# Optimization experiments

Hardware: AMD Instinct MI355X
Metric: run time of the kernel (lower is better)

Reference implementation:

```python
import jax, jax.numpy as jnp
import numpy as np

NUM_STEPS = 2  # consensus iterations


def psi3(r, edge_index, W3, b3):
    # one-layer message passing GNN: sum-aggregate neighbors, add self, linear, relu
    src, dst = edge_index[0], edge_index[1]
    agg = jnp.zeros_like(r).at[dst].add(r[src])
    return jax.nn.relu((r + agg) @ W3 + b3)


def setup_inputs() -> dict:
    key = jax.random.key(0)
    ks = jax.random.split(key, 12)
    N_total, C_in = 4096, 128   # global entity table
    N_s, N_t = 1024, 1024       # source / target graph sizes (B=1)
    E = 16384                   # edges per graph (avg degree 16)
    C1, C2 = 256, 256           # psi_1 / psi_2 output dims
    R = 32                      # psi_3 in_channels == out_channels
    s_in = 1.0 / np.sqrt(C_in)
    s_r = 1.0 / np.sqrt(R)
    inp = {}
    inp['inputs'] = jax.random.normal(ks[0], (N_total, C_in), jnp.float32)
    inp['index_n1'] = jax.random.randint(ks[1], (N_s,), 0, N_total)
    inp['index_n2'] = jax.random.randint(ks[2], (N_t,), 0, N_total)
    inp['edge_index_s'] = jax.random.randint(ks[3], (2, E), 0, N_s)
    inp['edge_index_t'] = jax.random.randint(ks[4], (2, E), 0, N_t)
    # psi_1 / psi_2: linear entity encoders
    inp['W1'] = jax.random.uniform(ks[5], (C_in, C1), jnp.float32, -s_in, s_in)
    inp['W2'] = jax.random.uniform(ks[6], (C_in, C2), jnp.float32, -s_in, s_in)
    # psi_3 weights
    inp['W3'] = jax.random.uniform(ks[7], (R, R), jnp.float32, -s_r, s_r)
    inp['b3'] = jnp.zeros((R,), jnp.float32)
    # consensus MLP: R -> R -> 1
    inp['Wm1'] = jax.random.uniform(ks[8], (R, R), jnp.float32, -s_r, s_r)
    inp['bm1'] = jnp.zeros((R,), jnp.float32)
    inp['Wm2'] = jax.random.uniform(ks[9], (R, 1), jnp.float32, -s_r, s_r)
    inp['bm2'] = jnp.zeros((1,), jnp.float32)
    # random node indicator functions r_s for each consensus step (drawn
    # with torch.randn inside the original forward; precomputed here)
    inp['rs_all'] = jax.random.normal(ks[10], (NUM_STEPS, N_s, R), jnp.float32)
    return inp


def reference(inputs, index_n1, index_n2, edge_index_s, edge_index_t,
              W1, W2, W3, b3, Wm1, bm1, Wm2, bm2, rs_all):
    time_emb = inputs @ W1  # psi_1
    rel_emb = inputs @ W2   # psi_2
    # h = cat(time, rel) per node; B=1 so masks are all-true
    h_s = jnp.concatenate([time_emb[index_n1], rel_emb[index_n1]], axis=-1)  # [N_s, C1+C2]
    h_t = jnp.concatenate([time_emb[index_n2], rel_emb[index_n2]], axis=-1)  # [N_t, C1+C2]
    S_hat = h_s @ h_t.T  # [N_s, N_t] dense similarity
    S_0 = jax.nn.softmax(S_hat, axis=-1)  # masked_softmax with full mask

    def step(S_hat, r_s):
        S = jax.nn.softmax(S_hat, axis=-1)
        r_t = S.T @ r_s                                  # [N_t, R]
        o_s = psi3(r_s, edge_index_s, W3, b3)            # [N_s, R]
        o_t = psi3(r_t, edge_index_t, W3, b3)            # [N_t, R]
        D = o_s[:, None, :] - o_t[None, :, :]            # [N_s, N_t, R]
        delta = (jax.nn.relu(D @ Wm1 + bm1) @ Wm2 + bm2)[..., 0]  # mlp(D).squeeze(-1)
        return S_hat + delta, None

    S_hat, _ = jax.lax.scan(step, S_hat, rs_all)
    S_L = jax.nn.softmax(S_hat, axis=-1)
    return S_0, S_L
```

## Files before the change

kernel.cpp:

```cpp
#include <hip/hip_runtime.h>
#include <math.h>

#define N_S   1024
#define N_T   1024
#define C_IN  128
#define E_EDG 16384
#define R     32
#define NSTEP 2

__global__ __launch_bounds__(256) void k_pre(const float* __restrict__ W1,
                                             const float* __restrict__ W2,
                                             float* __restrict__ G,
                                             float* __restrict__ zbuf) {
    int t = threadIdx.x;
    ((float4*)zbuf)[blockIdx.x * 256 + t] = make_float4(0.f, 0.f, 0.f, 0.f);

    int a = blockIdx.x;
    __shared__ float wa[512];
    __shared__ float wt[64][129];
    __shared__ float red[256];
    for (int s = t; s < 512; s += 256)
        wa[s] = (s < 256) ? W1[a * 256 + s] : W2[a * 256 + (s - 256)];
    __syncthreads();

    float acc = 0.f;
    int b = t & 127, h = t >> 7;
    for (int ci = 0; ci < 8; ++ci) {
        const float* Wsrc = (ci < 4) ? W1 : W2;
        int cbase = (ci < 4) ? ci * 64 : (ci - 4) * 64;
#pragma unroll
        for (int it = 0; it < 8; ++it) {
            int s = it * 256 + t;
            int br = s >> 4, q = s & 15;
            float4 v = *(const float4*)(Wsrc + (size_t)br * 256 + cbase + q * 4);
            wt[q * 4 + 0][br] = v.x; wt[q * 4 + 1][br] = v.y;
            wt[q * 4 + 2][br] = v.z; wt[q * 4 + 3][br] = v.w;
        }
        __syncthreads();
        const float* wac = wa + ci * 64 + h * 32;
#pragma unroll
        for (int cc = 0; cc < 32; ++cc)
            acc += wac[cc] * wt[h * 32 + cc][b];
        __syncthreads();
    }
    red[t] = acc;
    __syncthreads();
    if (t < 128) G[a * 128 + t] = red[t] + red[t + 128];
}

__global__ __launch_bounds__(128) void k_ys(const float* __restrict__ X,
                                            const int* __restrict__ idx1,
                                            const float* __restrict__ G,
                                            float* __restrict__ Ys) {
    int i = blockIdx.x;
    int a = threadIdx.x;
    __shared__ float x[128];
    int row = idx1[i];
    x[a] = X[row * 128 + a];
    __syncthreads();
    float acc = 0.f;
#pragma unroll 8
    for (int d = 0; d < 128; ++d)
        acc += x[d] * G[d * 128 + a];
    Ys[i * 128 + a] = acc;
}

__global__ __launch_bounds__(256) void k_shat(const float* __restrict__ Ys,
                                              const float* __restrict__ X,
                                              const int* __restrict__ idx2,
                                              float* __restrict__ Shat,
                                              float2* __restrict__ part) {
    __shared__ float As[64][132];
    __shared__ float Bs[64][132];
    const int i0 = blockIdx.y * 64, j0 = blockIdx.x * 64;
    const int t = threadIdx.x;
    for (int s = t; s < 64 * 32; s += 256) {
        int row = s >> 5, q = s & 31;
        float4 v = ((const float4*)(Ys + (size_t)(i0 + row) * 128))[q];
        *(float4*)&As[row][q * 4] = v;
    }
    for (int s = t; s < 64 * 32; s += 256) {
        int row = s >> 5, q = s & 31;
        int src = idx2[j0 + row];
        float4 v = ((const float4*)(X + (size_t)src * 128))[q];
        *(float4*)&Bs[row][q * 4] = v;
    }
    __syncthreads();
    const int r = t >> 4, c = t & 15;
    float acc[4][4] = {};
    for (int k = 0; k < 128; k += 4) {
        float4 ya[4], xb[4];
#pragma unroll
        for (int a = 0; a < 4; ++a) ya[a] = *(const float4*)&As[r + 16 * a][k];
#pragma unroll
        for (int b = 0; b < 4; ++b) xb[b] = *(const float4*)&Bs[c + 16 * b][k];
#pragma unroll
        for (int a = 0; a < 4; ++a)
#pragma unroll
            for (int b = 0; b < 4; ++b)
                acc[a][b] += ya[a].x * xb[b].x + ya[a].y * xb[b].y +
                             ya[a].z * xb[b].z + ya[a].w * xb[b].w;
    }
#pragma unroll
    for (int a = 0; a < 4; ++a) {
#pragma unroll
        for (int b = 0; b < 4; ++b)
            Shat[(size_t)(i0 + r + 16 * a) * 1024 + (j0 + c + 16 * b)] = acc[a][b];
        float M = fmaxf(fmaxf(acc[a][0], acc[a][1]), fmaxf(acc[a][2], acc[a][3]));
#pragma unroll
        for (int m = 1; m < 16; m <<= 1) M = fmaxf(M, __shfl_xor(M, m, 16));
        float Ss = 0.f;
#pragma unroll
        for (int b = 0; b < 4; ++b) Ss += __expf(acc[a][b] - M);
#pragma unroll
        for (int m = 1; m < 16; m <<= 1) Ss += __shfl_xor(Ss, m, 16);
        if (c == 0)
            part[(size_t)(i0 + r + 16 * a) * 16 + blockIdx.x] = make_float2(M, Ss);
    }
}

__global__ __launch_bounds__(256) void k_scat_s(const int* __restrict__ es,
                                                const float* __restrict__ rs_all,
                                                float* __restrict__ aggs0,
                                                float* __restrict__ aggs1) {
    int gid = blockIdx.x * 256 + threadIdx.x;
    int k = gid & 31;
    int ei = gid >> 5;
    int step = ei >> 14;
    int e = ei & (E_EDG - 1);
    int src = es[e], dst = es[E_EDG + e];
    const float* rs = rs_all + (size_t)step * N_S * R;
    float* aggs = step ? aggs1 : aggs0;
    atomicAdd(&aggs[(size_t)dst * 32 + k], rs[(size_t)src * 32 + k]);
}

__global__ __launch_bounds__(256) void k_post_s(const float* __restrict__ rs_all,
                                                const float* __restrict__ aggs0,
                                                const float* __restrict__ aggs1,
                                                const float* __restrict__ W3,
                                                const float* __restrict__ b3,
                                                const float* __restrict__ Wm1,
                                                const float* __restrict__ bm1,
                                                float* __restrict__ P0,
                                                float* __restrict__ P1) {
    __shared__ float w3[1024], wm1[1024];
    __shared__ float ul[8][33], ol[8][33];
    int t = threadIdx.x;
    for (int s = t; s < 1024; s += 256) { w3[s] = W3[s]; wm1[s] = Wm1[s]; }
    int row8 = t >> 5, k = t & 31;
    int grow = blockIdx.x * 8 + row8;
    int step = grow >> 10;
    int r = grow & 1023;
    const float* rs = rs_all + (size_t)step * N_S * R;
    const float* agg = step ? aggs1 : aggs0;
    float* P = step ? P1 : P0;
    ul[row8][k] = rs[(size_t)r * 32 + k] + agg[(size_t)r * 32 + k];
    __syncthreads();
    float acc = b3[k];
#pragma unroll
    for (int m = 0; m < 32; ++m) acc += ul[row8][m] * w3[m * 32 + k];
    ol[row8][k] = fmaxf(acc, 0.f);
    __syncthreads();
    float acc2 = bm1[k];
#pragma unroll
    for (int m = 0; m < 32; ++m) acc2 += ol[row8][m] * wm1[m * 32 + k];
    P[(size_t)r * 32 + k] = acc2;
}

__global__ __launch_bounds__(256) void k_rt(const float* __restrict__ Shat,
                                            const float2* __restrict__ part,
                                            const float* __restrict__ rs,
                                            float* __restrict__ rt,
                                            float* __restrict__ out0) {
    int j0 = blockIdx.x * 64;
    int i0 = blockIdx.y * 128;
    int t = threadIdx.x;
    __shared__ float Sl[16][68];
    __shared__ float Rl[16][36];
    __shared__ float mrow[128], irow[128];
    if (t < 128) {
        const float2* pr = part + (size_t)(i0 + t) * 16;
        float M = -1e30f, S = 0.f;
        float2 ps[16];
#pragma unroll
        for (int q = 0; q < 16; ++q) { ps[q] = pr[q]; M = fmaxf(M, ps[q].x); }
#pragma unroll
        for (int q = 0; q < 16; ++q) S += ps[q].y * __expf(ps[q].x - M);
        mrow[t] = M;
        irow[t] = 1.f / S;
    }
    __syncthreads();
    int k = t & 31, jg = t >> 5;
    float acc[8] = {};
    for (int ic = 0; ic < 128; ic += 16) {
        for (int s = t; s < 16 * 16; s += 256) {
            int row = s >> 4, q = s & 15;
            int lr = ic + row;
            float4 v = ((const float4*)(Shat + (size_t)(i0 + lr) * 1024 + j0))[q];
            float m = mrow[lr], inv = irow[lr];
            v.x = __expf(v.x - m) * inv;
            v.y = __expf(v.y - m) * inv;
            v.z = __expf(v.z - m) * inv;
            v.w = __expf(v.w - m) * inv;
            *(float4*)&Sl[row][q * 4] = v;
            if (out0)
                ((float4*)(out0 + (size_t)(i0 + lr) * 1024 + j0))[q] = v;
        }
        for (int s = t; s < 16 * 8; s += 256) {
            int row = s >> 3, q = s & 7;
            *(float4*)&Rl[row][q * 4] =
                ((const float4*)(rs + (size_t)(i0 + ic + row) * 32))[q];
        }
        __syncthreads();
#pragma unroll
        for (int ii = 0; ii < 16; ++ii) {
            float rv = Rl[ii][k];
#pragma unroll
            for (int m = 0; m < 8; ++m)
                acc[m] += Sl[ii][jg * 8 + m] * rv;
        }
        __syncthreads();
    }
#pragma unroll
    for (int m = 0; m < 8; ++m)
        atomicAdd(&rt[(size_t)(j0 + jg * 8 + m) * 32 + k], acc[m]);
}

__global__ __launch_bounds__(256) void k_scat_t(const int* __restrict__ et,
                                                const float* __restrict__ rt,
                                                float* __restrict__ aggt) {
    int gid = blockIdx.x * 256 + threadIdx.x;
    int k = gid & 31;
    int e = gid >> 5;
    int src = et[e], dst = et[E_EDG + e];
    atomicAdd(&aggt[(size_t)dst * 32 + k], rt[(size_t)src * 32 + k]);
}

__global__ __launch_bounds__(256) void k_post_t(const float* __restrict__ rt,
                                                const float* __restrict__ aggt,
                                                const float* __restrict__ W3,
                                                const float* __restrict__ b3,
                                                const float* __restrict__ Wm1,
                                                float* __restrict__ Q) {
    __shared__ float w3[1024], wm1[1024];
    __shared__ float ul[8][33], ol[8][33];
    int t = threadIdx.x;
    for (int s = t; s < 1024; s += 256) { w3[s] = W3[s]; wm1[s] = Wm1[s]; }
    int row8 = t >> 5, k = t & 31;
    int r = blockIdx.x * 8 + row8;
    ul[row8][k] = rt[(size_t)r * 32 + k] + aggt[(size_t)r * 32 + k];
    __syncthreads();
    float acc = b3[k];
#pragma unroll
    for (int m = 0; m < 32; ++m) acc += ul[row8][m] * w3[m * 32 + k];
    ol[row8][k] = fmaxf(acc, 0.f);
    __syncthreads();
    float acc2 = 0.f;
#pragma unroll
    for (int m = 0; m < 32; ++m) acc2 += ol[row8][m] * wm1[m * 32 + k];
    Q[(size_t)r * 32 + k] = acc2;
}

__global__ __launch_bounds__(256) void k_delta(const float* __restrict__ P,
                                               const float* __restrict__ Q,
                                               const float* __restrict__ Wm2,
                                               const float* __restrict__ bm2,
                                               float* __restrict__ Shat,
                                               float2* __restrict__ part,
                                               float* __restrict__ zbuf) {
    __shared__ float Pl[64][36], Ql[64][36];
    int t = threadIdx.x;
    if (blockIdx.y == 0) {
        float4 z = make_float4(0.f, 0.f, 0.f, 0.f);
        float4* zb = (float4*)zbuf;
        int base = (blockIdx.x * 256 + t) * 4;
#pragma unroll
        for (int q = 0; q < 4; ++q) zb[base + q] = z;
    }
    int i0 = blockIdx.y * 64, j0 = blockIdx.x * 64;
    for (int s = t; s < 64 * 8; s += 256) {
        int row = s >> 3, q = s & 7;
        *(float4*)&Pl[row][q * 4] = ((const float4*)(P + (size_t)(i0 + row) * 32))[q];
        *(float4*)&Ql[row][q * 4] = ((const float4*)(Q + (size_t)(j0 + row) * 32))[q];
    }
    __syncthreads();
    int r = t >> 4, c = t & 15;
    float bv = bm2[0];
    float acc[4][4] = {};
#pragma unroll
    for (int q = 0; q < 8; ++q) {
        float4 w = ((const float4*)Wm2)[q];
        float4 pa[4], qb[4];
#pragma unroll
        for (int a = 0; a < 4; ++a) pa[a] = *(const float4*)&Pl[r + 16 * a][q * 4];
#pragma unroll
        for (int b = 0; b < 4; ++b) qb[b] = *(const float4*)&Ql[c + 16 * b][q * 4];
#pragma unroll
        for (int a = 0; a < 4; ++a)
#pragma unroll
            for (int b = 0; b < 4; ++b)
                acc[a][b] += w.x * fmaxf(pa[a].x - qb[b].x, 0.f)
                           + w.y * fmaxf(pa[a].y - qb[b].y, 0.f)
                           + w.z * fmaxf(pa[a].z - qb[b].z, 0.f)
                           + w.w * fmaxf(pa[a].w - qb[b].w, 0.f);
    }
#pragma unroll
    for (int a = 0; a < 4; ++a) {
        float v[4];
#pragma unroll
        for (int b = 0; b < 4; ++b) {
            size_t idx = (size_t)(i0 + r + 16 * a) * 1024 + (j0 + c + 16 * b);
            v[b] = Shat[idx] + acc[a][b] + bv;
            Shat[idx] = v[b];
        }
        float M = fmaxf(fmaxf(v[0], v[1]), fmaxf(v[2], v[3]));
#pragma unroll
        for (int m = 1; m < 16; m <<= 1) M = fmaxf(M, __shfl_xor(M, m, 16));
        float Ss = 0.f;
#pragma unroll
        for (int b = 0; b < 4; ++b) Ss += __expf(v[b] - M);
#pragma unroll
        for (int m = 1; m < 16; m <<= 1) Ss += __shfl_xor(Ss, m, 16);
        if (c == 0)
            part[(size_t)(i0 + r + 16 * a) * 16 + blockIdx.x] = make_float2(M, Ss);
    }
}

__global__ __launch_bounds__(256) void k_fsm(const float* __restrict__ Shat,
                                             const float2* __restrict__ part,
                                             float* __restrict__ out2) {
    int i = blockIdx.x, t = threadIdx.x;
    const float2* pr = part + (size_t)i * 16;
    float M = -1e30f, S = 0.f;
    float2 ps[16];
#pragma unroll
    for (int q = 0; q < 16; ++q) { ps[q] = pr[q]; M = fmaxf(M, ps[q].x); }
#pragma unroll
    for (int q = 0; q < 16; ++q) S += ps[q].y * __expf(ps[q].x - M);
    float inv = 1.f / S;
    const float* row = Shat + (size_t)i * 1024;
#pragma unroll
    for (int j = 0; j < 4; ++j)
        out2[(size_t)i * 1024 + t + 256 * j] = __expf(row[t + 256 * j] - M) * inv;
}

extern "C" void kernel_launch(void* const* d_in, const int* in_sizes, int n_in,
                              void* d_out, int out_size, void* d_ws, size_t ws_size,
                              hipStream_t stream) {
    const float* inputs = (const float*)d_in[0];
    const int*   idx1   = (const int*)d_in[1];
    const int*   idx2   = (const int*)d_in[2];
    const int*   es     = (const int*)d_in[3];
    const int*   et     = (const int*)d_in[4];
    const float* W1     = (const float*)d_in[5];
    const float* W2     = (const float*)d_in[6];
    const float* W3     = (const float*)d_in[7];
    const float* b3     = (const float*)d_in[8];
    const float* Wm1    = (const float*)d_in[9];
    const float* bm1    = (const float*)d_in[10];
    const float* Wm2    = (const float*)d_in[11];
    const float* bm2    = (const float*)d_in[12];
    const float* rs_all = (const float*)d_in[13];
    float* out = (float*)d_out;
    float* ws  = (float*)d_ws;

    float*  Shat  = ws;
    float*  Ys    = Shat + (1 << 20);
    float*  G     = Ys + 131072;
    float2* part  = (float2*)(G + 16384);
    float*  rt    = G + 16384 + 32768;
    float*  aggt  = rt + 32768;
    float*  aggs0 = aggt + 32768;
    float*  aggs1 = aggs0 + 32768;
    float*  P0    = aggs1 + 32768;
    float*  P1    = P0 + 32768;
    float*  Q     = P1 + 32768;

    k_pre<<<128, 256, 0, stream>>>(W1, W2, G, rt);
    k_ys<<<1024, 128, 0, stream>>>(inputs, idx1, G, Ys);
    k_shat<<<dim3(16, 16), 256, 0, stream>>>(Ys, inputs, idx2, Shat, part);
    k_scat_s<<<4096, 256, 0, stream>>>(es, rs_all, aggs0, aggs1);
    k_post_s<<<256, 256, 0, stream>>>(rs_all, aggs0, aggs1, W3, b3, Wm1, bm1, P0, P1);

    for (int step = 0; step < NSTEP; ++step) {
        const float* rs = rs_all + (size_t)step * N_S * R;
        k_rt<<<dim3(16, 8), 256, 0, stream>>>(Shat, part, rs, rt,
                                              step == 0 ? out : nullptr);
        k_scat_t<<<2048, 256, 0, stream>>>(et, rt, aggt);
        k_post_t<<<128, 256, 0, stream>>>(rt, aggt, W3, b3, Wm1, Q);
        k_delta<<<dim3(16, 16), 256, 0, stream>>>(step ? P1 : P0, Q, Wm2, bm2,
                                                  Shat, part, rt);
    }
    k_fsm<<<1024, 256, 0, stream>>>(Shat, part, out + (1 << 20));
}
```

Before: 182.1 us.

## Fuse setup and per-step GNN stages into fewer kernels with redundant recompute

The separate Ys, S_hat, source scatter and source post-processing kernels are merged into one k_build kernel. Each block recomputes its 64-row Ys tile in shared memory and performs a strided share of the source-edge atomics. Each step's target scatter, psi3 and MLP-first-layer stages move into k_delta: every block filters the target edges for its 64 columns into a shared edge list, aggregates them with shared-memory atomics, and recomputes P and Q locally. The goal is to cut the launch count roughly in half and drop several global round trips. The cost is redundant recomputation of Ys, P and Q across blocks, a full edge scan in every delta block, and a separate rt buffer per step zeroed by extra blocks in k_pre.

```diff
diff --git a/kernel.cpp b/kernel.cpp
--- a/kernel.cpp
+++ b/kernel.cpp
@@ -3,7 +3,6 @@
 
 #define N_S   1024
 #define N_T   1024
-#define C_IN  128
 #define E_EDG 16384
 #define R     32
 #define NSTEP 2
@@ -12,22 +11,23 @@
                                              const float* __restrict__ W2,
                                              float* __restrict__ G,
                                              float* __restrict__ zbuf) {
-    int t = threadIdx.x;
-    ((float4*)zbuf)[blockIdx.x * 256 + t] = make_float4(0.f, 0.f, 0.f, 0.f);
-
-    int a = blockIdx.x;
+    const int t = threadIdx.x, bid = blockIdx.x;
+    if (bid >= 128) {
+        ((float4*)zbuf)[(bid - 128) * 256 + t] = make_float4(0.f, 0.f, 0.f, 0.f);
+        return;
+    }
     __shared__ float wa[512];
     __shared__ float wt[64][129];
     __shared__ float red[256];
+    const int a = bid;
     for (int s = t; s < 512; s += 256)
         wa[s] = (s < 256) ? W1[a * 256 + s] : W2[a * 256 + (s - 256)];
     __syncthreads();
-
     float acc = 0.f;
-    int b = t & 127, h = t >> 7;
+    const int b = t & 127, h = t >> 7;
     for (int ci = 0; ci < 8; ++ci) {
         const float* Wsrc = (ci < 4) ? W1 : W2;
-        int cbase = (ci < 4) ? ci * 64 : (ci - 4) * 64;
+        const int cbase = (ci & 3) * 64;
 #pragma unroll
         for (int it = 0; it < 8; ++it) {
             int s = it * 256 + t;
@@ -48,123 +48,91 @@
     if (t < 128) G[a * 128 + t] = red[t] + red[t + 128];
 }
 
-__global__ __launch_bounds__(128) void k_ys(const float* __restrict__ X,
-                                            const int* __restrict__ idx1,
-                                            const float* __restrict__ G,
-                                            float* __restrict__ Ys) {
-    int i = blockIdx.x;
-    int a = threadIdx.x;
-    __shared__ float x[128];
-    int row = idx1[i];
-    x[a] = X[row * 128 + a];
-    __syncthreads();
-    float acc = 0.f;
-#pragma unroll 8
-    for (int d = 0; d < 128; ++d)
-        acc += x[d] * G[d * 128 + a];
-    Ys[i * 128 + a] = acc;
-}
-
-__global__ __launch_bounds__(256) void k_shat(const float* __restrict__ Ys,
-                                              const float* __restrict__ X,
-                                              const int* __restrict__ idx2,
-                                              float* __restrict__ Shat,
-                                              float2* __restrict__ part) {
+__global__ __launch_bounds__(256) void k_build(
+    const float* __restrict__ X, const int* __restrict__ idx1,
+    const int* __restrict__ idx2, const int* __restrict__ es,
+    const float* __restrict__ rs_all, const float* __restrict__ G,
+    float* aggs0, float* aggs1,
+    float* __restrict__ Shat, float2* __restrict__ part) {
     __shared__ float As[64][132];
-    __shared__ float Bs[64][132];
-    const int i0 = blockIdx.y * 64, j0 = blockIdx.x * 64;
-    const int t = threadIdx.x;
+    union U { float Xs[64][128]; float Bs[64][132]; };
+    __shared__ U u;
+    const int t = threadIdx.x, bid = blockIdx.x;
+    const int i0 = (bid >> 4) * 64, j0 = (bid & 15) * 64, jt = bid & 15;
+
+    for (int v = bid * 256 + t; v < 2 * E_EDG * 32; v += 65536) {
+        int k = v & 31, ei = v >> 5;
+        int step = ei >> 14, e = ei & (E_EDG - 1);
+        int src = es[e], dst = es[E_EDG + e];
+        const float* rs = rs_all + (size_t)step * N_S * R;
+        float* aggs = step ? aggs1 : aggs0;
+        atomicAdd(&aggs[(size_t)dst * 32 + k], rs[(size_t)src * 32 + k]);
+    }
+
     for (int s = t; s < 64 * 32; s += 256) {
         int row = s >> 5, q = s & 31;
-        float4 v = ((const float4*)(Ys + (size_t)(i0 + row) * 128))[q];
-        *(float4*)&As[row][q * 4] = v;
-    }
+        *(float4*)&u.Xs[row][q * 4] =
+            ((const float4*)(X + (size_t)idx1[i0 + row] * 128))[q];
+    }
+    __syncthreads();
+
+    {
+        const int a = t & 127, h = t >> 7;
+        float acc[32];
+#pragma unroll
+        for (int r = 0; r < 32; ++r) acc[r] = 0.f;
+        for (int dq = 0; dq < 32; ++dq) {
+            const float* gp = G + dq * 4 * 128 + a;
+            float g0 = gp[0], g1 = gp[128], g2 = gp[256], g3 = gp[384];
+#pragma unroll
+            for (int r = 0; r < 32; ++r) {
+                float4 x = *(const float4*)&u.Xs[h * 32 + r][dq * 4];
+                acc[r] += x.x * g0 + x.y * g1 + x.z * g2 + x.w * g3;
+            }
+        }
+#pragma unroll
+        for (int r = 0; r < 32; ++r) As[h * 32 + r][a] = acc[r];
+    }
+    __syncthreads();
+
     for (int s = t; s < 64 * 32; s += 256) {
         int row = s >> 5, q = s & 31;
-        int src = idx2[j0 + row];
-        float4 v = ((const float4*)(X + (size_t)src * 128))[q];
-        *(float4*)&Bs[row][q * 4] = v;
-    }
-    __syncthreads();
+        *(float4*)&u.Bs[row][q * 4] =
+            ((const float4*)(X + (size_t)idx2[j0 + row] * 128))[q];
+    }
+    __syncthreads();
+
     const int r = t >> 4, c = t & 15;
     float acc[4][4] = {};
     for (int k = 0; k < 128; k += 4) {
         float4 ya[4], xb[4];
 #pragma unroll
-        for (int a = 0; a < 4; ++a) ya[a] = *(const float4*)&As[r + 16 * a][k];
-#pragma unroll
-        for (int b = 0; b < 4; ++b) xb[b] = *(const float4*)&Bs[c + 16 * b][k];
-#pragma unroll
-        for (int a = 0; a < 4; ++a)
-#pragma unroll
-            for (int b = 0; b < 4; ++b)
-                acc[a][b] += ya[a].x * xb[b].x + ya[a].y * xb[b].y +
-                             ya[a].z * xb[b].z + ya[a].w * xb[b].w;
-    }
-#pragma unroll
-    for (int a = 0; a < 4; ++a) {
-#pragma unroll
-        for (int b = 0; b < 4; ++b)
-            Shat[(size_t)(i0 + r + 16 * a) * 1024 + (j0 + c + 16 * b)] = acc[a][b];
-        float M = fmaxf(fmaxf(acc[a][0], acc[a][1]), fmaxf(acc[a][2], acc[a][3]));
+        for (int a2 = 0; a2 < 4; ++a2) ya[a2] = *(const float4*)&As[r + 16 * a2][k];
+#pragma unroll
+        for (int b2 = 0; b2 < 4; ++b2) xb[b2] = *(const float4*)&u.Bs[c + 16 * b2][k];
+#pragma unroll
+        for (int a2 = 0; a2 < 4; ++a2)
+#pragma unroll
+            for (int b2 = 0; b2 < 4; ++b2)
+                acc[a2][b2] += ya[a2].x * xb[b2].x + ya[a2].y * xb[b2].y +
+                               ya[a2].z * xb[b2].z + ya[a2].w * xb[b2].w;
+    }
+#pragma unroll
+    for (int a2 = 0; a2 < 4; ++a2) {
+#pragma unroll
+        for (int b2 = 0; b2 < 4; ++b2)
+            Shat[(size_t)(i0 + r + 16 * a2) * 1024 + (j0 + c + 16 * b2)] = acc[a2][b2];
+        float M = fmaxf(fmaxf(acc[a2][0], acc[a2][1]), fmaxf(acc[a2][2], acc[a2][3]));
 #pragma unroll
         for (int m = 1; m < 16; m <<= 1) M = fmaxf(M, __shfl_xor(M, m, 16));
         float Ss = 0.f;
 #pragma unroll
-        for (int b = 0; b < 4; ++b) Ss += __expf(acc[a][b] - M);
+        for (int b2 = 0; b2 < 4; ++b2) Ss += __expf(acc[a2][b2] - M);
 #pragma unroll
         for (int m = 1; m < 16; m <<= 1) Ss += __shfl_xor(Ss, m, 16);
         if (c == 0)
-            part[(size_t)(i0 + r + 16 * a) * 16 + blockIdx.x] = make_float2(M, Ss);
-    }
-}
-
-__global__ __launch_bounds__(256) void k_scat_s(const int* __restrict__ es,
-                                                const float* __restrict__ rs_all,
-                                                float* __restrict__ aggs0,
-                                                float* __restrict__ aggs1) {
-    int gid = blockIdx.x * 256 + threadIdx.x;
-    int k = gid & 31;
-    int ei = gid >> 5;
-    int step = ei >> 14;
-    int e = ei & (E_EDG - 1);
-    int src = es[e], dst = es[E_EDG + e];
-    const float* rs = rs_all + (size_t)step * N_S * R;
-    float* aggs = step ? aggs1 : aggs0;
-    atomicAdd(&aggs[(size_t)dst * 32 + k], rs[(size_t)src * 32 + k]);
-}
-
-__global__ __launch_bounds__(256) void k_post_s(const float* __restrict__ rs_all,
-                                                const float* __restrict__ aggs0,
-                                                const float* __restrict__ aggs1,
-                                                const float* __restrict__ W3,
-                                                const float* __restrict__ b3,
-                                                const float* __restrict__ Wm1,
-                                                const float* __restrict__ bm1,
-                                                float* __restrict__ P0,
-                                                float* __restrict__ P1) {
-    __shared__ float w3[1024], wm1[1024];
-    __shared__ float ul[8][33], ol[8][33];
-    int t = threadIdx.x;
-    for (int s = t; s < 1024; s += 256) { w3[s] = W3[s]; wm1[s] = Wm1[s]; }
-    int row8 = t >> 5, k = t & 31;
-    int grow = blockIdx.x * 8 + row8;
-    int step = grow >> 10;
-    int r = grow & 1023;
-    const float* rs = rs_all + (size_t)step * N_S * R;
-    const float* agg = step ? aggs1 : aggs0;
-    float* P = step ? P1 : P0;
-    ul[row8][k] = rs[(size_t)r * 32 + k] + agg[(size_t)r * 32 + k];
-    __syncthreads();
-    float acc = b3[k];
-#pragma unroll
-    for (int m = 0; m < 32; ++m) acc += ul[row8][m] * w3[m * 32 + k];
-    ol[row8][k] = fmaxf(acc, 0.f);
-    __syncthreads();
-    float acc2 = bm1[k];
-#pragma unroll
-    for (int m = 0; m < 32; ++m) acc2 += ol[row8][m] * wm1[m * 32 + k];
-    P[(size_t)r * 32 + k] = acc2;
+            part[(size_t)(i0 + r + 16 * a2) * 16 + jt] = make_float2(M, Ss);
+    }
 }
 
 __global__ __launch_bounds__(256) void k_rt(const float* __restrict__ Shat,
@@ -226,66 +194,78 @@
         atomicAdd(&rt[(size_t)(j0 + jg * 8 + m) * 32 + k], acc[m]);
 }
 
-__global__ __launch_bounds__(256) void k_scat_t(const int* __restrict__ et,
-                                                const float* __restrict__ rt,
-                                                float* __restrict__ aggt) {
-    int gid = blockIdx.x * 256 + threadIdx.x;
-    int k = gid & 31;
-    int e = gid >> 5;
-    int src = et[e], dst = et[E_EDG + e];
-    atomicAdd(&aggt[(size_t)dst * 32 + k], rt[(size_t)src * 32 + k]);
-}
-
-__global__ __launch_bounds__(256) void k_post_t(const float* __restrict__ rt,
-                                                const float* __restrict__ aggt,
-                                                const float* __restrict__ W3,
-                                                const float* __restrict__ b3,
-                                                const float* __restrict__ Wm1,
-                                                float* __restrict__ Q) {
+__global__ __launch_bounds__(256) void k_delta(
+    const float* __restrict__ rs, const float* __restrict__ aggs,
+    const float* __restrict__ rt, const int* __restrict__ et,
+    const float* __restrict__ W3, const float* __restrict__ b3,
+    const float* __restrict__ Wm1, const float* __restrict__ bm1,
+    const float* __restrict__ Wm2, const float* __restrict__ bm2,
+    float* __restrict__ Shat, float2* __restrict__ part) {
     __shared__ float w3[1024], wm1[1024];
-    __shared__ float ul[8][33], ol[8][33];
-    int t = threadIdx.x;
+    __shared__ float us[64][33], rq[64][33], agg[64][33];
+    __shared__ float Pl[64][36], Ql[64][36];
+    __shared__ ushort2 elist[2048];
+    __shared__ int ecnt;
+    const int t = threadIdx.x;
+    const int bx = blockIdx.x, by = blockIdx.y;
+    const int i0 = by * 64, j0 = bx * 64;
+
     for (int s = t; s < 1024; s += 256) { w3[s] = W3[s]; wm1[s] = Wm1[s]; }
-    int row8 = t >> 5, k = t & 31;
-    int r = blockIdx.x * 8 + row8;
-    ul[row8][k] = rt[(size_t)r * 32 + k] + aggt[(size_t)r * 32 + k];
-    __syncthreads();
-    float acc = b3[k];
-#pragma unroll
-    for (int m = 0; m < 32; ++m) acc += ul[row8][m] * w3[m * 32 + k];
-    ol[row8][k] = fmaxf(acc, 0.f);
-    __syncthreads();
-    float acc2 = 0.f;
-#pragma unroll
-    for (int m = 0; m < 32; ++m) acc2 += ol[row8][m] * wm1[m * 32 + k];
-    Q[(size_t)r * 32 + k] = acc2;
-}
-
-__global__ __launch_bounds__(256) void k_delta(const float* __restrict__ P,
-                                               const float* __restrict__ Q,
-                                               const float* __restrict__ Wm2,
-                                               const float* __restrict__ bm2,
-                                               float* __restrict__ Shat,
-                                               float2* __restrict__ part,
-                                               float* __restrict__ zbuf) {
-    __shared__ float Pl[64][36], Ql[64][36];
-    int t = threadIdx.x;
-    if (blockIdx.y == 0) {
-        float4 z = make_float4(0.f, 0.f, 0.f, 0.f);
-        float4* zb = (float4*)zbuf;
-        int base = (blockIdx.x * 256 + t) * 4;
-#pragma unroll
-        for (int q = 0; q < 4; ++q) zb[base + q] = z;
-    }
-    int i0 = blockIdx.y * 64, j0 = blockIdx.x * 64;
+    if (t == 0) ecnt = 0;
     for (int s = t; s < 64 * 8; s += 256) {
         int row = s >> 3, q = s & 7;
-        *(float4*)&Pl[row][q * 4] = ((const float4*)(P + (size_t)(i0 + row) * 32))[q];
-        *(float4*)&Ql[row][q * 4] = ((const float4*)(Q + (size_t)(j0 + row) * 32))[q];
-    }
-    __syncthreads();
-    int r = t >> 4, c = t & 15;
-    float bv = bm2[0];
+        float4 a4 = ((const float4*)(rs + (size_t)(i0 + row) * 32))[q];
+        float4 b4 = ((const float4*)(aggs + (size_t)(i0 + row) * 32))[q];
+        a4.x += b4.x; a4.y += b4.y; a4.z += b4.z; a4.w += b4.w;
+        *(float4*)&us[row][q * 4] = a4;
+        *(float4*)&rq[row][q * 4] = ((const float4*)(rt + (size_t)(j0 + row) * 32))[q];
+        *(float4*)&agg[row][q * 4] = make_float4(0.f, 0.f, 0.f, 0.f);
+    }
+    __syncthreads();
+
+    for (int e = t; e < E_EDG; e += 256) {
+        int dst = et[E_EDG + e];
+        if ((dst >> 6) == bx) {
+            int p = atomicAdd(&ecnt, 1);
+            if (p < 2048)
+                elist[p] = make_ushort2((unsigned short)et[e],
+                                        (unsigned short)(dst & 63));
+        }
+    }
+    __syncthreads();
+
+    const int k = t & 31, team = t >> 5;
+    const int ne = (ecnt < 2048) ? ecnt : 2048;
+    for (int idx = team; idx < ne; idx += 8) {
+        ushort2 ed = elist[idx];
+        atomicAdd(&agg[ed.y][k], rt[(size_t)ed.x * 32 + k]);
+    }
+    __syncthreads();
+
+    const float b3k = b3[k], bm1k = bm1[k];
+    for (int p = 0; p < 8; ++p) {
+        const int row = p * 8 + team;
+        float acc = b3k;
+#pragma unroll
+        for (int m = 0; m < 32; ++m) acc += us[row][m] * w3[m * 32 + k];
+        float o = fmaxf(acc, 0.f);
+        float pv = bm1k;
+#pragma unroll
+        for (int m = 0; m < 32; ++m) pv += __shfl(o, m, 32) * wm1[m * 32 + k];
+        Pl[row][k] = pv;
+        float acc2 = b3k;
+#pragma unroll
+        for (int m = 0; m < 32; ++m) acc2 += (rq[row][m] + agg[row][m]) * w3[m * 32 + k];
+        float o2 = fmaxf(acc2, 0.f);
+        float qv = 0.f;
+#pragma unroll
+        for (int m = 0; m < 32; ++m) qv += __shfl(o2, m, 32) * wm1[m * 32 + k];
+        Ql[row][k] = qv;
+    }
+    __syncthreads();
+
+    const int r = t >> 4, c = t & 15;
+    const float bv = bm2[0];
     float acc[4][4] = {};
 #pragma unroll
     for (int q = 0; q < 8; ++q) {
@@ -322,7 +302,7 @@
 #pragma unroll
         for (int m = 1; m < 16; m <<= 1) Ss += __shfl_xor(Ss, m, 16);
         if (c == 0)
-            part[(size_t)(i0 + r + 16 * a) * 16 + blockIdx.x] = make_float2(M, Ss);
+            part[(size_t)(i0 + r + 16 * a) * 16 + bx] = make_float2(M, Ss);
     }
 }
 
@@ -365,31 +345,25 @@
     float* ws  = (float*)d_ws;
 
     float*  Shat  = ws;
-    float*  Ys    = Shat + (1 << 20);
-    float*  G     = Ys + 131072;
+    float*  G     = Shat + (1 << 20);
     float2* part  = (float2*)(G + 16384);
-    float*  rt    = G + 16384 + 32768;
-    float*  aggt  = rt + 32768;
-    float*  aggs0 = aggt + 32768;
+    float*  rt0   = G + 16384 + 32768;
+    float*  rt1   = rt0 + 32768;
+    float*  aggs0 = rt1 + 32768;
     float*  aggs1 = aggs0 + 32768;
-    float*  P0    = aggs1 + 32768;
-    float*  P1    = P0 + 32768;
-    float*  Q     = P1 + 32768;
-
-    k_pre<<<128, 256, 0, stream>>>(W1, W2, G, rt);
-    k_ys<<<1024, 128, 0, stream>>>(inputs, idx1, G, Ys);
-    k_shat<<<dim3(16, 16), 256, 0, stream>>>(Ys, inputs, idx2, Shat, part);
-    k_scat_s<<<4096, 256, 0, stream>>>(es, rs_all, aggs0, aggs1);
-    k_post_s<<<256, 256, 0, stream>>>(rs_all, aggs0, aggs1, W3, b3, Wm1, bm1, P0, P1);
-
+
+    k_pre<<<256, 256, 0, stream>>>(W1, W2, G, rt0);
+    k_build<<<256, 256, 0, stream>>>(inputs, idx1, idx2, es, rs_all, G,
+                                     aggs0, aggs1, Shat, part);
     for (int step = 0; step < NSTEP; ++step) {
-        const float* rs = rs_all + (size_t)step * N_S * R;
-        k_rt<<<dim3(16, 8), 256, 0, stream>>>(Shat, part, rs, rt,
+        const float* rs   = rs_all + (size_t)step * N_S * R;
+        float*       rtS  = step ? rt1 : rt0;
+        const float* aggS = step ? aggs1 : aggs0;
+        k_rt<<<dim3(16, 8), 256, 0, stream>>>(Shat, part, rs, rtS,
                                               step == 0 ? out : nullptr);
-        k_scat_t<<<2048, 256, 0, stream>>>(et, rt, aggt);
-        k_post_t<<<128, 256, 0, stream>>>(rt, aggt, W3, b3, Wm1, Q);
-        k_delta<<<dim3(16, 16), 256, 0, stream>>>(step ? P1 : P0, Q, Wm2, bm2,
-                                                  Shat, part, rt);
+        k_delta<<<dim3(16, 16), 256, 0, stream>>>(rs, aggS, rtS, et,
+                                                  W3, b3, Wm1, bm1, Wm2, bm2,
+                                                  Shat, part);
     }
     k_fsm<<<1024, 256, 0, stream>>>(Shat, part, out + (1 << 20));
 }
```

New measurement: 358.8 us. +97.0%, slower.
